# Kernel tuning notes

Measured on AMD Instinct MI355X. Metric: run time of the kernel, lower is better.

## Reference

```python
import jax, jax.numpy as jnp
import numpy as np

N_NODES = 50000
N_EDGES = 1600000
IN_CH = 128
HEADS = 4
OUT_PER_HEAD = 32  # out_channels // heads with concat=True
NEG_SLOPE = 0.2    # GATConv default leaky_relu slope
SOFTMAX_EPS = 1e-16  # PyG scatter-softmax denominator eps
LN_EPS = 1e-5


def setup_inputs() -> dict:
    key = jax.random.key(0)
    ks = jax.random.split(key, 8)
    x = jax.random.normal(ks[0], (N_NODES, IN_CH), dtype=jnp.float32)
    edge_index = jax.random.randint(ks[1], (2, N_EDGES), 0, N_NODES, dtype=jnp.int32)
    W = jax.random.normal(ks[2], (IN_CH, HEADS * OUT_PER_HEAD), dtype=jnp.float32) * (1.0 / np.sqrt(IN_CH))
    att_src = jax.random.normal(ks[3], (HEADS, OUT_PER_HEAD), dtype=jnp.float32) * 0.1
    att_dst = jax.random.normal(ks[4], (HEADS, OUT_PER_HEAD), dtype=jnp.float32) * 0.1
    bias = jnp.zeros((HEADS * OUT_PER_HEAD,), dtype=jnp.float32)
    gamma = jnp.ones((HEADS * OUT_PER_HEAD,), dtype=jnp.float32)
    beta = jnp.zeros((HEADS * OUT_PER_HEAD,), dtype=jnp.float32)
    return {"x": x, "edge_index": edge_index, "W": W, "att_src": att_src,
            "att_dst": att_dst, "bias": bias, "gamma": gamma, "beta": beta}


def reference(x, edge_index, W, att_src, att_dst, bias, gamma, beta):
    N = x.shape[0]
    H, C = att_src.shape
    # GATConv default add_self_loops=True
    loop = jnp.arange(N, dtype=edge_index.dtype)
    src = jnp.concatenate([edge_index[0], loop])  # message source j
    dst = jnp.concatenate([edge_index[1], loop])  # aggregation target i

    h = (x @ W).reshape(N, H, C)                      # [N,H,C]
    a_s = jnp.einsum('nhc,hc->nh', h, att_src)        # [N,H]
    a_d = jnp.einsum('nhc,hc->nh', h, att_dst)        # [N,H]

    logits = jax.nn.leaky_relu(a_s[src] + a_d[dst], NEG_SLOPE)  # [E,H]
    # segment softmax over edges grouped by destination node
    m = jax.ops.segment_max(logits, dst, num_segments=N)        # [N,H]
    m = jnp.where(jnp.isfinite(m), m, 0.0)
    e = jnp.exp(logits - m[dst])
    s = jax.ops.segment_sum(e, dst, num_segments=N)             # [N,H]
    alpha = e / (s[dst] + SOFTMAX_EPS)                          # [E,H]

    msg = h[src] * alpha[:, :, None]                            # [E,H,C]
    out = jax.ops.segment_sum(msg, dst, num_segments=N)         # [N,H,C]
    out = out.reshape(N, H * C) + bias

    mu = out.mean(axis=-1, keepdims=True)
    var = ((out - mu) ** 2).mean(axis=-1, keepdims=True)
    y = (out - mu) / jnp.sqrt(var + LN_EPS) * gamma + beta
    return jax.nn.elu(y)
```

## Files before the change

### kernel.cpp

```cpp
#include <hip/hip_runtime.h>
#include <hip/hip_bf16.h>

typedef __hip_bfloat16 bf16;
typedef unsigned int u32;
typedef unsigned short u16;

constexpr int N   = 50000;
constexpr int E   = 1600000;
constexpr int C   = 128;
constexpr int H   = 4;
constexpr int NB  = 782;
constexpr int CAP = 2560;
constexpr int CHUNK = 4096;
constexpr float NEG  = 0.2f;
constexpr float SEPS = 1e-16f;
constexpr float LEPS = 1e-5f;

__device__ __forceinline__ float lo16(u32 v) { return __uint_as_float(v << 16); }
__device__ __forceinline__ float hi16(u32 v) { return __uint_as_float(v & 0xFFFF0000u); }

__global__ __launch_bounds__(256) void k1_gemm(
    const float* __restrict__ x, const float* __restrict__ W,
    const float* __restrict__ att_s, const float* __restrict__ att_d,
    bf16* __restrict__ hb, float* __restrict__ as_, float* __restrict__ ad_)
{
    const int nb = blockIdx.x * 16;
    const int t  = threadIdx.x;
    __shared__ float sx[16 * 128];
    const float4* xg = (const float4*)(x + nb * 128);
    ((float4*)sx)[t]       = xg[t];
    ((float4*)sx)[t + 256] = xg[t + 256];
    __syncthreads();

    const int c = t & 127;
    const int g = t >> 7;
    const float* xb = sx + (g << 10);
    float acc[8] = {0.f, 0.f, 0.f, 0.f, 0.f, 0.f, 0.f, 0.f};

    for (int k = 0; k < 128; k += 4) {
        const float w0 = W[(k + 0) * 128 + c];
        const float w1 = W[(k + 1) * 128 + c];
        const float w2 = W[(k + 2) * 128 + c];
        const float w3 = W[(k + 3) * 128 + c];
#pragma unroll
        for (int j = 0; j < 8; ++j) {
            const float4 xv = *(const float4*)(xb + j * 128 + k);
            acc[j] = fmaf(xv.x, w0, fmaf(xv.y, w1, fmaf(xv.z, w2, fmaf(xv.w, w3, acc[j]))));
        }
    }

    const int lane = t & 63;
    const int head = c >> 5;
    const float asc = att_s[c], adc = att_d[c];
#pragma unroll
    for (int j = 0; j < 8; ++j) {
        const int node = nb + (g << 3) + j;
        hb[node * 128 + c] = __float2bfloat16(acc[j]);
        float vs = acc[j] * asc;
        float vd = acc[j] * adc;
#pragma unroll
        for (int off = 16; off; off >>= 1) {
            vs += __shfl_xor(vs, off, 64);
            vd += __shfl_xor(vd, off, 64);
        }
        if ((lane & 31) == 0) {
            as_[node * H + head] = vs;
            ad_[node * H + head] = vd;
        }
    }
}

__global__ __launch_bounds__(256) void kbin(
    const int* __restrict__ ei, u32* __restrict__ gcur, u32* __restrict__ pairs)
{
    __shared__ u32 lcnt[NB], lbase[NB], lfill[NB];
    const int t = threadIdx.x;
    const int base = blockIdx.x * CHUNK;
    const int nE = min(CHUNK, E - base);
    for (int i = t; i < NB; i += 256) lcnt[i] = 0;
    __syncthreads();
    for (int i = t; i < nE; i += 256)
        atomicAdd(&lcnt[((u32)ei[E + base + i]) >> 6], 1u);
    __syncthreads();
    for (int i = t; i < NB; i += 256) {
        u32 cb = lcnt[i];
        lbase[i] = cb ? atomicAdd(&gcur[i], cb) : 0u;
        lfill[i] = 0u;
    }
    __syncthreads();
    for (int i = t; i < nE; i += 256) {
        u32 src = (u32)ei[base + i];
        u32 dst = (u32)ei[E + base + i];
        u32 b = dst >> 6;
        u32 pos = atomicAdd(&lfill[b], 1u);
        pairs[(size_t)b * CAP + lbase[b] + pos] = src | ((dst & 63u) << 16);
    }
}

__global__ __launch_bounds__(64) void kscan(
    const u32* __restrict__ gcur, u32* __restrict__ bbase, int* __restrict__ row_ptr)
{
    const int t = threadIdx.x;
    u32 vals[13];
    u32 s = 0;
#pragma unroll
    for (int i = 0; i < 13; ++i) {
        int idx = t * 13 + i;
        u32 v = (idx < NB) ? gcur[idx] : 0u;
        vals[i] = s; s += v;
    }
    u32 incl = s;
#pragma unroll
    for (int off = 1; off < 64; off <<= 1) {
        u32 u = __shfl_up(incl, off, 64);
        if (t >= off) incl += u;
    }
    const u32 excl = incl - s;
#pragma unroll
    for (int i = 0; i < 13; ++i) {
        int idx = t * 13 + i;
        if (idx < NB) bbase[idx] = excl + vals[i];
    }
    if (t == 0) row_ptr[N] = E;
}

__global__ __launch_bounds__(256) void kfill2(
    const u32* __restrict__ pairs, const u32* __restrict__ gcur,
    const u32* __restrict__ bbase, int* __restrict__ row_ptr, u16* __restrict__ col)
{
    __shared__ int jcnt[64], joff[64], jcur[64];
    const int b = blockIdx.x, t = threadIdx.x;
    const int cntb = (int)gcur[b];
    const int base = (int)bbase[b];
    if (t < 64) jcnt[t] = 0;
    __syncthreads();
    const u32* pr = pairs + (size_t)b * CAP;
    for (int i = t; i < cntb; i += 256) atomicAdd(&jcnt[pr[i] >> 16], 1);
    __syncthreads();
    if (t < 64) {
        int v = jcnt[t], incl = v;
#pragma unroll
        for (int off = 1; off < 64; off <<= 1) {
            int u = __shfl_up(incl, off, 64);
            if (t >= off) incl += u;
        }
        joff[t] = incl - v;
        const int n = b * 64 + t;
        if (n < N) row_ptr[n] = base + joff[t];
        jcur[t] = 0;
    }
    __syncthreads();
    for (int i = t; i < cntb; i += 256) {
        const u32 p = pr[i];
        const int j = p >> 16;
        const int pos = atomicAdd(&jcur[j], 1);
        col[base + joff[j] + pos] = (u16)(p & 0xFFFFu);
    }
}

__global__ __launch_bounds__(256) void kd_agg_ln(
    const int* __restrict__ row_ptr, const u16* __restrict__ col,
    const u32* __restrict__ hb, const float* __restrict__ as_,
    const float* __restrict__ ad_,
    const float* __restrict__ bias, const float* __restrict__ gamma,
    const float* __restrict__ beta, float* __restrict__ out)
{
    __shared__ float wlds[4][64];
    const int tid  = threadIdx.x;
    const int lane = tid & 63;
    const int wv   = __builtin_amdgcn_readfirstlane(tid >> 6);
    const int n    = __builtin_amdgcn_readfirstlane((int)blockIdx.x * 4 + (tid >> 6));
    if (n >= N) return;

    const int head  = lane >> 4;
    const int eoff  = lane & 15;
    const int wbase = head << 4;
    float* __restrict__ wrow = wlds[wv];

    const float adn = ad_[n * H + head];
    const float asn = as_[n * H + head];

    float ls = asn + adn;
    ls = fmaxf(ls, NEG * ls);
    const float wself = __expf(ls);
    float den = (eoff == 0) ? wself : 0.f;
    const u32 hvs = hb[n * 64 + lane];
    float num0 = wself * lo16(hvs);
    float num1 = wself * hi16(hvs);

    const int k0  = row_ptr[n];
    const int deg = row_ptr[n + 1] - k0;
    const int ntiles = (deg + 15) >> 4;

    const int cnt0 = deg < 16 ? deg : 16;
    const int cnt1 = (deg - 16) < 16 ? (deg - 16) : 16;
    int colv_cur = (eoff < cnt0) ? (int)col[k0 + eoff]      : 0;
    int colv_nxt = (eoff < cnt1) ? (int)col[k0 + 16 + eoff] : 0;
    float a_cur  = as_[colv_cur * H + head];
    int cntc = cnt0, cntn = cnt1;

    int k = k0;
    for (int t = 0; t < ntiles; ++t, k += 16) {
        const int rem2 = deg - 16 * (t + 2);
        const int cnt2 = rem2 < 16 ? rem2 : 16;
        const int cf_raw = (int)col[k + 32 + eoff];
        const int colv_f = (eoff < cnt2) ? cf_raw : 0;

        float le = a_cur + adn;
        le = fmaxf(le, NEG * le);
        const float w = (eoff < cntc) ? __expf(le) : 0.f;
        den += w;
        wrow[lane] = w;
        const int colc = colv_cur;

#define GL(i) const u32* rp##i = hb + ((size_t)(u32)__builtin_amdgcn_readlane(colc, i) << 6); \
              const u32 v##i = rp##i[lane];
        GL(0) GL(1) GL(2) GL(3) GL(4) GL(5) GL(6) GL(7)
        GL(8) GL(9) GL(10) GL(11) GL(12) GL(13) GL(14) GL(15)
#undef GL
        __builtin_amdgcn_sched_barrier(0);

        const float a_n = as_[colv_nxt * H + head];
        __builtin_amdgcn_sched_barrier(0);

        {
            const float4 wa = *(const float4*)(wrow + wbase + 0);
            num0 = fmaf(wa.x, lo16(v0), num0);  num1 = fmaf(wa.x, hi16(v0), num1);
            num0 = fmaf(wa.y, lo16(v1), num0);  num1 = fmaf(wa.y, hi16(v1), num1);
            num0 = fmaf(wa.z, lo16(v2), num0);  num1 = fmaf(wa.z, hi16(v2), num1);
            num0 = fmaf(wa.w, lo16(v3), num0);  num1 = fmaf(wa.w, hi16(v3), num1);
            const float4 wb = *(const float4*)(wrow + wbase + 4);
            num0 = fmaf(wb.x, lo16(v4), num0);  num1 = fmaf(wb.x, hi16(v4), num1);
            num0 = fmaf(wb.y, lo16(v5), num0);  num1 = fmaf(wb.y, hi16(v5), num1);
            num0 = fmaf(wb.z, lo16(v6), num0);  num1 = fmaf(wb.z, hi16(v6), num1);
            num0 = fmaf(wb.w, lo16(v7), num0);  num1 = fmaf(wb.w, hi16(v7), num1);
            const float4 wc = *(const float4*)(wrow + wbase + 8);
            num0 = fmaf(wc.x, lo16(v8), num0);  num1 = fmaf(wc.x, hi16(v8), num1);
            num0 = fmaf(wc.y, lo16(v9), num0);  num1 = fmaf(wc.y, hi16(v9), num1);
            num0 = fmaf(wc.z, lo16(v10), num0); num1 = fmaf(wc.z, hi16(v10), num1);
            num0 = fmaf(wc.w, lo16(v11), num0); num1 = fmaf(wc.w, hi16(v11), num1);
            const float4 wd = *(const float4*)(wrow + wbase + 12);
            num0 = fmaf(wd.x, lo16(v12), num0); num1 = fmaf(wd.x, hi16(v12), num1);
            num0 = fmaf(wd.y, lo16(v13), num0); num1 = fmaf(wd.y, hi16(v13), num1);
            num0 = fmaf(wd.z, lo16(v14), num0); num1 = fmaf(wd.z, hi16(v14), num1);
            num0 = fmaf(wd.w, lo16(v15), num0); num1 = fmaf(wd.w, hi16(v15), num1);
        }

        colv_cur = colv_nxt; colv_nxt = colv_f;
        a_cur = a_n;
        cntc = cntn; cntn = cnt2;
    }

#pragma unroll
    for (int off = 1; off < 16; off <<= 1) den += __shfl_xor(den, off, 64);

    const int c0 = lane * 2;
    const float inv_den = 1.f / (den + SEPS);
    const float2 bi = *(const float2*)(bias + c0);
    float v0 = num0 * inv_den + bi.x;
    float v1 = num1 * inv_den + bi.y;

    float sum = v0 + v1;
#pragma unroll
    for (int off = 32; off; off >>= 1) sum += __shfl_xor(sum, off, 64);
    const float mu = sum * (1.0f / C);
    const float d0 = v0 - mu, d1 = v1 - mu;
    float sq = d0 * d0 + d1 * d1;
#pragma unroll
    for (int off = 32; off; off >>= 1) sq += __shfl_xor(sq, off, 64);
    const float inv = rsqrtf(sq * (1.0f / C) + LEPS);
    const float2 ga = *(const float2*)(gamma + c0);
    const float2 be = *(const float2*)(beta  + c0);
    float y0 = d0 * inv * ga.x + be.x;
    float y1 = d1 * inv * ga.y + be.y;
    y0 = y0 > 0.f ? y0 : __expf(y0) - 1.f;
    y1 = y1 > 0.f ? y1 : __expf(y1) - 1.f;
    float2 o; o.x = y0; o.y = y1;
    *(float2*)(out + (size_t)n * C + c0) = o;
}

extern "C" void kernel_launch(void* const* d_in, const int* in_sizes, int n_in,
                              void* d_out, int out_size, void* d_ws, size_t ws_size,
                              hipStream_t stream)
{
    const float* x     = (const float*)d_in[0];
    const int*   ei    = (const int*)  d_in[1];
    const float* W     = (const float*)d_in[2];
    const float* att_s = (const float*)d_in[3];
    const float* att_d = (const float*)d_in[4];
    const float* bias  = (const float*)d_in[5];
    const float* gamma = (const float*)d_in[6];
    const float* beta  = (const float*)d_in[7];
    float* out = (float*)d_out;

    char* p = (char*)d_ws;
    bf16*  hb      = (bf16*)p;   p += (size_t)N * C * sizeof(bf16);
    float* as_     = (float*)p;  p += (size_t)N * H * sizeof(float);
    float* ad_     = (float*)p;  p += (size_t)N * H * sizeof(float);
    u32*   pairs   = (u32*)p;    p += (size_t)NB * CAP * sizeof(u32);
    u16*   col     = (u16*)p;    p += ((size_t)(E + 64) * sizeof(u16) + 15) & ~(size_t)15;
    int*   row_ptr = (int*)p;    p += ((size_t)(N + 1) * sizeof(int) + 15) & ~(size_t)15;
    u32*   gcur    = (u32*)p;    p += (size_t)NB * sizeof(u32);
    u32*   bbase   = (u32*)p;

    hipMemsetAsync(gcur, 0, NB * sizeof(u32), stream);
    k1_gemm<<<N / 16, 256, 0, stream>>>(x, W, att_s, att_d, hb, as_, ad_);
    kbin<<<(E + CHUNK - 1) / CHUNK, 256, 0, stream>>>(ei, gcur, pairs);
    kscan<<<1, 64, 0, stream>>>(gcur, bbase, row_ptr);
    kfill2<<<NB, 256, 0, stream>>>(pairs, gcur, bbase, row_ptr, col);
    kd_agg_ln<<<(N * 64) / 256, 256, 0, stream>>>(
        row_ptr, col, (const u32*)hb, as_, ad_, bias, gamma, beta, out);
}
```

Baseline: 231.7 us.

## Use split-bf16 MFMA for projection GEMM, stage kfill2 in LDS, enlarge bin chunks

Replaces the scalar FP32 projection GEMM with a matrix-core kernel. Inputs and weights are split into bf16 high and low parts, and three MFMA products per step recover near-FP32 accuracy. A new prep kernel transposes and splits W each call. kfill2 now stages pairs and the sorted column indices in shared memory so the global column writes are coalesced, and the binning chunk size grows so fewer blocks are launched. The cost is an extra kernel launch and higher LDS use per block.

```diff
diff --git a/kernel.cpp b/kernel.cpp
--- a/kernel.cpp
+++ b/kernel.cpp
@@ -4,6 +4,8 @@
 typedef __hip_bfloat16 bf16;
 typedef unsigned int u32;
 typedef unsigned short u16;
+typedef __attribute__((ext_vector_type(8))) short bf16x8;
+typedef __attribute__((ext_vector_type(4))) float f32x4;
 
 constexpr int N   = 50000;
 constexpr int E   = 1600000;
@@ -11,61 +13,139 @@
 constexpr int H   = 4;
 constexpr int NB  = 782;
 constexpr int CAP = 2560;
-constexpr int CHUNK = 4096;
+constexpr int CHUNK = 6250;
 constexpr float NEG  = 0.2f;
 constexpr float SEPS = 1e-16f;
 constexpr float LEPS = 1e-5f;
 
 __device__ __forceinline__ float lo16(u32 v) { return __uint_as_float(v << 16); }
 __device__ __forceinline__ float hi16(u32 v) { return __uint_as_float(v & 0xFFFF0000u); }
-
-__global__ __launch_bounds__(256) void k1_gemm(
-    const float* __restrict__ x, const float* __restrict__ W,
+__device__ __forceinline__ u16 bfbits(float f) {
+    __hip_bfloat16 h = __float2bfloat16(f);
+    return *reinterpret_cast<u16*>(&h);
+}
+
+__global__ __launch_bounds__(256) void k0_wprep(
+    const float* __restrict__ W, u16* __restrict__ wt_hi, u16* __restrict__ wt_lo)
+{
+    const int i = blockIdx.x * 256 + threadIdx.x;
+    const int c = i >> 7, k = i & 127;
+    const float w = W[k * 128 + c];
+    const __hip_bfloat16 h = __float2bfloat16(w);
+    const float fh = __bfloat162float(h);
+    wt_hi[i] = *(const u16*)&h;
+    wt_lo[i] = bfbits(w - fh);
+}
+
+__global__ __launch_bounds__(256) void k1_mfma(
+    const float* __restrict__ x,
+    const u16* __restrict__ wt_hi, const u16* __restrict__ wt_lo,
     const float* __restrict__ att_s, const float* __restrict__ att_d,
-    bf16* __restrict__ hb, float* __restrict__ as_, float* __restrict__ ad_)
-{
-    const int nb = blockIdx.x * 16;
+    u16* __restrict__ hb, float* __restrict__ as_, float* __restrict__ ad_)
+{
+    constexpr int LDX = 136;
+    __shared__ u16 xhi[64 * LDX];
+    __shared__ u16 xlo[64 * LDX];
     const int t  = threadIdx.x;
-    __shared__ float sx[16 * 128];
-    const float4* xg = (const float4*)(x + nb * 128);
-    ((float4*)sx)[t]       = xg[t];
-    ((float4*)sx)[t + 256] = xg[t + 256];
-    __syncthreads();
-
-    const int c = t & 127;
-    const int g = t >> 7;
-    const float* xb = sx + (g << 10);
-    float acc[8] = {0.f, 0.f, 0.f, 0.f, 0.f, 0.f, 0.f, 0.f};
-
-    for (int k = 0; k < 128; k += 4) {
-        const float w0 = W[(k + 0) * 128 + c];
-        const float w1 = W[(k + 1) * 128 + c];
-        const float w2 = W[(k + 2) * 128 + c];
-        const float w3 = W[(k + 3) * 128 + c];
-#pragma unroll
-        for (int j = 0; j < 8; ++j) {
-            const float4 xv = *(const float4*)(xb + j * 128 + k);
-            acc[j] = fmaf(xv.x, w0, fmaf(xv.y, w1, fmaf(xv.z, w2, fmaf(xv.w, w3, acc[j]))));
-        }
-    }
+    const int m0 = blockIdx.x * 64;
+
+#pragma unroll
+    for (int it = 0; it < 8; ++it) {
+        const int idx = it * 1024 + t * 4;
+        const int r = idx >> 7, c = idx & 127;
+        const int gr = min(m0 + r, N - 1);
+        const float4 v = *(const float4*)(x + (size_t)gr * 128 + c);
+        ushort4 sh, sl;
+        {
+            __hip_bfloat16 h0 = __float2bfloat16(v.x);
+            __hip_bfloat16 h1 = __float2bfloat16(v.y);
+            __hip_bfloat16 h2 = __float2bfloat16(v.z);
+            __hip_bfloat16 h3 = __float2bfloat16(v.w);
+            sh.x = *(u16*)&h0; sh.y = *(u16*)&h1; sh.z = *(u16*)&h2; sh.w = *(u16*)&h3;
+            sl.x = bfbits(v.x - __bfloat162float(h0));
+            sl.y = bfbits(v.y - __bfloat162float(h1));
+            sl.z = bfbits(v.z - __bfloat162float(h2));
+            sl.w = bfbits(v.w - __bfloat162float(h3));
+        }
+        *(ushort4*)(xhi + r * LDX + c) = sh;
+        *(ushort4*)(xlo + r * LDX + c) = sl;
+    }
+    __syncthreads();
 
     const int lane = t & 63;
-    const int head = c >> 5;
-    const float asc = att_s[c], adc = att_d[c];
-#pragma unroll
-    for (int j = 0; j < 8; ++j) {
-        const int node = nb + (g << 3) + j;
-        hb[node * 128 + c] = __float2bfloat16(acc[j]);
-        float vs = acc[j] * asc;
-        float vd = acc[j] * adc;
-#pragma unroll
-        for (int off = 16; off; off >>= 1) {
-            vs += __shfl_xor(vs, off, 64);
-            vd += __shfl_xor(vd, off, 64);
-        }
-        if ((lane & 31) == 0) {
-            as_[node * H + head] = vs;
-            ad_[node * H + head] = vd;
+    const int w    = t >> 6;
+    const int arow = w * 16 + (lane & 15);
+    const int akg  = lane >> 4;
+    const int bcol = lane & 15;
+    const int aq   = lane >> 4;
+
+    bf16x8 Ah[4], Al[4];
+#pragma unroll
+    for (int ks = 0; ks < 4; ++ks) {
+        Ah[ks] = *(const bf16x8*)(xhi + arow * LDX + ks * 32 + akg * 8);
+        Al[ks] = *(const bf16x8*)(xlo + arow * LDX + ks * 32 + akg * 8);
+    }
+
+    f32x4 acc[8];
+#pragma unroll
+    for (int nt = 0; nt < 8; ++nt) acc[nt] = f32x4{0.f, 0.f, 0.f, 0.f};
+
+#pragma unroll
+    for (int nt = 0; nt < 8; ++nt) {
+        const u16* bp = wt_hi + (nt * 16 + bcol) * 128 + akg * 8;
+        const u16* bq = wt_lo + (nt * 16 + bcol) * 128 + akg * 8;
+#pragma unroll
+        for (int ks = 0; ks < 4; ++ks) {
+            const bf16x8 Bh = *(const bf16x8*)(bp + ks * 32);
+            const bf16x8 Bl = *(const bf16x8*)(bq + ks * 32);
+            acc[nt] = __builtin_amdgcn_mfma_f32_16x16x32_bf16(Ah[ks], Bh, acc[nt], 0, 0, 0);
+            acc[nt] = __builtin_amdgcn_mfma_f32_16x16x32_bf16(Al[ks], Bh, acc[nt], 0, 0, 0);
+            acc[nt] = __builtin_amdgcn_mfma_f32_16x16x32_bf16(Ah[ks], Bl, acc[nt], 0, 0, 0);
+        }
+    }
+
+#pragma unroll
+    for (int nt = 0; nt < 8; ++nt) {
+        const int ch = nt * 16 + bcol;
+#pragma unroll
+        for (int r = 0; r < 4; ++r) {
+            const int node = m0 + w * 16 + aq * 4 + r;
+            if (node < N) hb[(size_t)node * 128 + ch] = bfbits(acc[nt][r]);
+        }
+    }
+
+    float ps[4][4], pd[4][4];
+#pragma unroll
+    for (int h = 0; h < 4; ++h) {
+        const float a0 = att_s[32 * h + bcol],      a1 = att_s[32 * h + 16 + bcol];
+        const float d0 = att_d[32 * h + bcol],      d1 = att_d[32 * h + 16 + bcol];
+#pragma unroll
+        for (int r = 0; r < 4; ++r) {
+            ps[h][r] = acc[2 * h][r] * a0 + acc[2 * h + 1][r] * a1;
+            pd[h][r] = acc[2 * h][r] * d0 + acc[2 * h + 1][r] * d1;
+        }
+    }
+#pragma unroll
+    for (int off = 1; off < 16; off <<= 1) {
+#pragma unroll
+        for (int h = 0; h < 4; ++h)
+#pragma unroll
+            for (int r = 0; r < 4; ++r) {
+                ps[h][r] += __shfl_xor(ps[h][r], off, 64);
+                pd[h][r] += __shfl_xor(pd[h][r], off, 64);
+            }
+    }
+    if (bcol == 0) {
+#pragma unroll
+        for (int r = 0; r < 4; ++r) {
+            const int node = m0 + w * 16 + aq * 4 + r;
+            if (node < N) {
+#pragma unroll
+                for (int h = 0; h < 4; ++h) {
+                    as_[node * H + h] = ps[h][r];
+                    ad_[node * H + h] = pd[h][r];
+                }
+            }
         }
     }
 }
@@ -128,14 +208,17 @@
     const u32* __restrict__ pairs, const u32* __restrict__ gcur,
     const u32* __restrict__ bbase, int* __restrict__ row_ptr, u16* __restrict__ col)
 {
+    __shared__ u32 spr[CAP];
+    __shared__ u16 scol[CAP];
     __shared__ int jcnt[64], joff[64], jcur[64];
     const int b = blockIdx.x, t = threadIdx.x;
     const int cntb = (int)gcur[b];
     const int base = (int)bbase[b];
     if (t < 64) jcnt[t] = 0;
-    __syncthreads();
     const u32* pr = pairs + (size_t)b * CAP;
-    for (int i = t; i < cntb; i += 256) atomicAdd(&jcnt[pr[i] >> 16], 1);
+    for (int i = t; i < cntb; i += 256) spr[i] = pr[i];
+    __syncthreads();
+    for (int i = t; i < cntb; i += 256) atomicAdd(&jcnt[spr[i] >> 16], 1);
     __syncthreads();
     if (t < 64) {
         int v = jcnt[t], incl = v;
@@ -151,11 +234,13 @@
     }
     __syncthreads();
     for (int i = t; i < cntb; i += 256) {
-        const u32 p = pr[i];
+        const u32 p = spr[i];
         const int j = p >> 16;
         const int pos = atomicAdd(&jcur[j], 1);
-        col[base + joff[j] + pos] = (u16)(p & 0xFFFFu);
-    }
+        scol[joff[j] + pos] = (u16)(p & 0xFFFFu);
+    }
+    __syncthreads();
+    for (int i = t; i < cntb; i += 256) col[base + i] = scol[i];
 }
 
 __global__ __launch_bounds__(256) void kd_agg_ln(
@@ -301,11 +386,15 @@
     u16*   col     = (u16*)p;    p += ((size_t)(E + 64) * sizeof(u16) + 15) & ~(size_t)15;
     int*   row_ptr = (int*)p;    p += ((size_t)(N + 1) * sizeof(int) + 15) & ~(size_t)15;
     u32*   gcur    = (u32*)p;    p += (size_t)NB * sizeof(u32);
-    u32*   bbase   = (u32*)p;
+    u32*   bbase   = (u32*)p;    p += (((size_t)NB * sizeof(u32)) + 15) & ~(size_t)15;
+    u16*   wt_hi   = (u16*)p;    p += (size_t)128 * 128 * sizeof(u16);
+    u16*   wt_lo   = (u16*)p;
 
     hipMemsetAsync(gcur, 0, NB * sizeof(u32), stream);
-    k1_gemm<<<N / 16, 256, 0, stream>>>(x, W, att_s, att_d, hb, as_, ad_);
-    kbin<<<(E + CHUNK - 1) / CHUNK, 256, 0, stream>>>(ei, gcur, pairs);
+    k0_wprep<<<64, 256, 0, stream>>>(W, wt_hi, wt_lo);
+    k1_mfma<<<(N + 63) / 64, 256, 0, stream>>>(x, wt_hi, wt_lo, att_s, att_d,
+                                               (u16*)hb, as_, ad_);
+    kbin<<<E / CHUNK, 256, 0, stream>>>(ei, gcur, pairs);
     kscan<<<1, 64, 0, stream>>>(gcur, bbase, row_ptr);
     kfill2<<<NB, 256, 0, stream>>>(pairs, gcur, bbase, row_ptr, col);
     kd_agg_ln<<<(N * 64) / 256, 256, 0, stream>>>(
```

New measurement: 223.7 us. 1.04x faster.
